# Kernel tuning notes

Measured on AMD Instinct MI355X. Metric: run time of the kernel, lower is better.

The kernel has to match this reference:

```python
import jax, jax.numpy as jnp
import numpy as np

N_NODES = 50000
N_EDGES = 800000
IN_DIM = 128
HID_DIM = 128
N_CLASSES = 40


def setup_inputs() -> dict:
    key = jax.random.key(0)
    ks = jax.random.split(key, 12)
    s = 0.05
    inp = {
        "X": jax.random.normal(ks[0], (N_NODES, IN_DIM), jnp.float32),
        "A": jax.random.randint(ks[1], (2, N_EDGES), 0, N_NODES, dtype=jnp.int64),
        "W0": jax.random.normal(ks[2], (HID_DIM, IN_DIM), jnp.float32) * s,
        "b0": jnp.zeros((HID_DIM,), jnp.float32),
        "W1": jax.random.normal(ks[3], (HID_DIM, HID_DIM), jnp.float32) * s,
        "b1": jnp.zeros((HID_DIM,), jnp.float32),
        "W2": jax.random.normal(ks[4], (HID_DIM, HID_DIM), jnp.float32) * s,
        "b2": jnp.zeros((HID_DIM,), jnp.float32),
        "W3": jax.random.normal(ks[5], (HID_DIM, HID_DIM), jnp.float32) * s,
        "b3": jnp.zeros((HID_DIM,), jnp.float32),
        "Wf": jax.random.normal(ks[6], (N_CLASSES, HID_DIM), jnp.float32) * s,
        "bf": jnp.zeros((N_CLASSES,), jnp.float32),
    }
    return inp


def _gcn_conv(x, W, b, src, dst):
    # FrobeniusNormGCNConv: normalize weight by Frobenius norm, then standard GCNConv
    Wn = W / jnp.linalg.norm(W)
    h = x @ Wn.T  # [N, out]
    # gcn_norm with self-loops (edge weight 1.0): deg over targets + 1 self loop
    ones = jnp.ones((dst.shape[0],), h.dtype)
    deg = jax.ops.segment_sum(ones, dst, num_segments=N_NODES) + 1.0
    dinv = jax.lax.rsqrt(deg)  # [N]
    norm = dinv[src] * dinv[dst]  # [E]
    # scatter-add of normalized source messages into targets
    agg = jax.ops.segment_sum(norm[:, None] * h[src], dst, num_segments=N_NODES)
    # self-loop contribution: dinv[i]^2 * h[i]; bias added after aggregation
    return agg + (dinv * dinv)[:, None] * h + b


def reference(X, A, W0, b0, W1, b1, W2, b2, W3, b3, Wf, bf):
    src, dst = A[0], A[1]
    h = _gcn_conv(X, W0, b0, src, dst)
    skip = h
    for W, b in ((W1, b1), (W2, b2), (W3, b3)):
        h = _gcn_conv(h, W, b, src, dst)
        h = jax.nn.relu(h)
        h = h + skip  # residual skip (dropout identity in eval mode)
        skip = h
    return h @ Wf.T + bf
```

## Files before the change

### kernel.cpp

```cpp
#include <hip/hip_runtime.h>

#define N_NODES_C 50000
#define N_EDGES_C 800000
#define DIM 128
#define NCLS 40
#define SCAN_NB ((N_NODES_C + 255) / 256)

typedef __attribute__((ext_vector_type(8))) short bf16x8;
typedef __attribute__((ext_vector_type(4))) float f32x4;

__device__ inline float bf2f(unsigned short u) {
    union { unsigned int i; float f; } c;
    c.i = ((unsigned int)u) << 16;
    return c.f;
}
__device__ inline unsigned short f2bf(float f) {
    union { float f; unsigned int i; } c;
    c.f = f;
    unsigned int x = c.i;
    x += 0x7fffu + ((x >> 16) & 1u);
    return (unsigned short)(x >> 16);
}
__device__ inline void add4b(float4& a, const ushort4& u) {
    a.x += bf2f(u.x);
    a.y += bf2f(u.y);
    a.z += bf2f(u.z);
    a.w += bf2f(u.w);
}

__global__ __launch_bounds__(256) void k_scales(const float* __restrict__ W0,
                                                const float* __restrict__ W1,
                                                const float* __restrict__ W2,
                                                const float* __restrict__ W3,
                                                float* __restrict__ scale_inv) {
    const float* W = blockIdx.x == 0 ? W0 : blockIdx.x == 1 ? W1 : blockIdx.x == 2 ? W2 : W3;
    float s = 0.f;
    for (int i = threadIdx.x; i < DIM * DIM; i += 256) {
        float v = W[i];
        s += v * v;
    }
    #pragma unroll
    for (int off = 32; off >= 1; off >>= 1) s += __shfl_down(s, off);
    __shared__ float red[4];
    int lane = threadIdx.x & 63, wid = threadIdx.x >> 6;
    if (lane == 0) red[wid] = s;
    __syncthreads();
    if (threadIdx.x == 0) {
        float tot = red[0] + red[1] + red[2] + red[3];
        scale_inv[blockIdx.x] = 1.0f / sqrtf(tot);
    }
}

__global__ __launch_bounds__(256) void k_f2b(const float* __restrict__ in,
                                             unsigned short* __restrict__ outb, int n4) {
    int i = blockIdx.x * 256 + threadIdx.x;
    if (i >= n4) return;
    float4 v = reinterpret_cast<const float4*>(in)[i];
    reinterpret_cast<ushort4*>(outb)[i] =
        make_ushort4(f2bf(v.x), f2bf(v.y), f2bf(v.z), f2bf(v.w));
}

__global__ __launch_bounds__(256) void k_w2b(const float* __restrict__ W0,
                                             const float* __restrict__ W1,
                                             const float* __restrict__ W2,
                                             const float* __restrict__ W3,
                                             unsigned short* __restrict__ Wb) {
    int m = blockIdx.x >> 4;
    int idx = (blockIdx.x & 15) * 256 + threadIdx.x;
    const float* W = m == 0 ? W0 : m == 1 ? W1 : m == 2 ? W2 : W3;
    float4 v = reinterpret_cast<const float4*>(W)[idx];
    reinterpret_cast<ushort4*>(Wb + (size_t)m * DIM * DIM)[idx] =
        make_ushort4(f2bf(v.x), f2bf(v.y), f2bf(v.z), f2bf(v.w));
}

__global__ void k_deg(const int* __restrict__ A, int* __restrict__ cnt, int E) {
    int e = blockIdx.x * 256 + threadIdx.x;
    if (e >= E) return;
    atomicAdd(&cnt[A[E + e]], 1);
}

__global__ __launch_bounds__(256) void k_scan_part(const int* __restrict__ cnt,
                                                   int* __restrict__ partial,
                                                   float* __restrict__ dinv, int n) {
    int idx = blockIdx.x * 256 + threadIdx.x;
    int v = (idx < n) ? cnt[idx] : 0;
    if (idx < n) dinv[idx] = rsqrtf((float)v + 1.0f);
    int s = v;
    #pragma unroll
    for (int off = 32; off >= 1; off >>= 1) s += __shfl_down(s, off);
    __shared__ int red[4];
    int lane = threadIdx.x & 63, wid = threadIdx.x >> 6;
    if (lane == 0) red[wid] = s;
    __syncthreads();
    if (threadIdx.x == 0) partial[blockIdx.x] = red[0] + red[1] + red[2] + red[3];
}

__global__ __launch_bounds__(256) void k_scan_mid(const int* __restrict__ partial,
                                                  int* __restrict__ base,
                                                  int* __restrict__ ptr, int nb, int n) {
    int tid = threadIdx.x;
    int v = (tid < nb) ? partial[tid] : 0;
    int lane = tid & 63, wid = tid >> 6;
    int sc = v;
    #pragma unroll
    for (int off = 1; off < 64; off <<= 1) {
        int t = __shfl_up(sc, off);
        if (lane >= off) sc += t;
    }
    __shared__ int wsum[4], wpre[4];
    if (lane == 63) wsum[wid] = sc;
    __syncthreads();
    if (tid == 0) {
        int acc = 0;
        #pragma unroll
        for (int w = 0; w < 4; ++w) { wpre[w] = acc; acc += wsum[w]; }
    }
    __syncthreads();
    int excl = wpre[wid] + sc - v;
    if (tid < nb) base[tid] = excl;
    if (tid == 255) ptr[n] = wpre[3] + sc;
}

__global__ __launch_bounds__(256) void k_scan_final(const int* __restrict__ cnt,
                                                    const int* __restrict__ base,
                                                    int* __restrict__ ptr, int n) {
    int idx = blockIdx.x * 256 + threadIdx.x;
    int v = (idx < n) ? cnt[idx] : 0;
    int tid = threadIdx.x, lane = tid & 63, wid = tid >> 6;
    int sc = v;
    #pragma unroll
    for (int off = 1; off < 64; off <<= 1) {
        int t = __shfl_up(sc, off);
        if (lane >= off) sc += t;
    }
    __shared__ int wsum[4], wpre[4];
    if (lane == 63) wsum[wid] = sc;
    __syncthreads();
    if (tid == 0) {
        int acc = 0;
        #pragma unroll
        for (int w = 0; w < 4; ++w) { wpre[w] = acc; acc += wsum[w]; }
    }
    __syncthreads();
    if (idx < n) ptr[idx] = base[blockIdx.x] + wpre[wid] + sc - v;
}

__global__ void k_fill(const int* __restrict__ A, const int* __restrict__ ptr,
                       int* __restrict__ fill, int* __restrict__ esrc, int E) {
    int e = blockIdx.x * 256 + threadIdx.x;
    if (e >= E) return;
    int s = A[e];
    int d = A[E + e];
    int pos = ptr[d] + atomicAdd(&fill[d], 1);
    esrc[pos] = s;
}

__global__ __launch_bounds__(256) void k_gemm_mfma(const unsigned short* __restrict__ Xb,
                                                   const unsigned short* __restrict__ Wb,
                                                   const float* __restrict__ scale_ptr,
                                                   const float* __restrict__ dinv,
                                                   unsigned short* __restrict__ Gb, int N) {
    int tid = threadIdx.x;
    int w = tid >> 6;
    int l = tid & 63;
    int l15 = l & 15;
    int lg = l >> 4;
    int arow = blockIdx.x * 64 + w * 16 + l15;
    if (arow >= N) arow = N - 1;
    float scale = scale_ptr[0];

    f32x4 acc[8];
    #pragma unroll
    for (int ct = 0; ct < 8; ++ct) acc[ct] = f32x4{0.f, 0.f, 0.f, 0.f};

    #pragma unroll
    for (int kc = 0; kc < 4; ++kc) {
        int ko = kc * 32 + lg * 8;
        bf16x8 a = *reinterpret_cast<const bf16x8*>(&Xb[(size_t)arow * DIM + ko]);
        #pragma unroll
        for (int ct = 0; ct < 8; ++ct) {
            bf16x8 b = *reinterpret_cast<const bf16x8*>(&Wb[(size_t)(ct * 16 + l15) * DIM + ko]);
            acc[ct] = __builtin_amdgcn_mfma_f32_16x16x32_bf16(a, b, acc[ct], 0, 0, 0);
        }
    }
    int outrow0 = blockIdx.x * 64 + w * 16 + lg * 4;
    #pragma unroll
    for (int r = 0; r < 4; ++r) {
        int row = outrow0 + r;
        if (row < N) {
            float dv = dinv[row] * scale;
            #pragma unroll
            for (int ct = 0; ct < 8; ++ct)
                Gb[(size_t)row * DIM + ct * 16 + l15] = f2bf(acc[ct][r] * dv);
        }
    }
}

__global__ __launch_bounds__(256) void k_agg(const unsigned short* __restrict__ Gb,
                                             const float* __restrict__ bias,
                                             const float* __restrict__ dinv,
                                             const int* __restrict__ ptr,
                                             const int* __restrict__ esrc,
                                             const unsigned short* __restrict__ skipb,
                                             unsigned short* __restrict__ outb,
                                             int relu_res, int N) {
    int n = blockIdx.x * 8 + (threadIdx.x >> 5);
    if (n >= N) return;
    int l = threadIdx.x & 31;
    const ushort4* __restrict__ Gv = reinterpret_cast<const ushort4*>(Gb);
    int beg = ptr[n], end = ptr[n + 1];
    float4 a0 = make_float4(0.f, 0.f, 0.f, 0.f), a1 = a0, a2 = a0, a3 = a0;
    int e = beg;
    for (; e + 8 <= end; e += 8) {
        int s0 = esrc[e + 0], s1 = esrc[e + 1], s2 = esrc[e + 2], s3 = esrc[e + 3];
        int s4 = esrc[e + 4], s5 = esrc[e + 5], s6 = esrc[e + 6], s7 = esrc[e + 7];
        ushort4 g0 = Gv[(size_t)s0 * 32 + l];
        ushort4 g1 = Gv[(size_t)s1 * 32 + l];
        ushort4 g2 = Gv[(size_t)s2 * 32 + l];
        ushort4 g3 = Gv[(size_t)s3 * 32 + l];
        ushort4 g4 = Gv[(size_t)s4 * 32 + l];
        ushort4 g5 = Gv[(size_t)s5 * 32 + l];
        ushort4 g6 = Gv[(size_t)s6 * 32 + l];
        ushort4 g7 = Gv[(size_t)s7 * 32 + l];
        add4b(a0, g0);
        add4b(a1, g1);
        add4b(a2, g2);
        add4b(a3, g3);
        add4b(a0, g4);
        add4b(a1, g5);
        add4b(a2, g6);
        add4b(a3, g7);
    }
    for (; e + 4 <= end; e += 4) {
        int s0 = esrc[e + 0], s1 = esrc[e + 1], s2 = esrc[e + 2], s3 = esrc[e + 3];
        ushort4 g0 = Gv[(size_t)s0 * 32 + l];
        ushort4 g1 = Gv[(size_t)s1 * 32 + l];
        ushort4 g2 = Gv[(size_t)s2 * 32 + l];
        ushort4 g3 = Gv[(size_t)s3 * 32 + l];
        add4b(a0, g0);
        add4b(a1, g1);
        add4b(a2, g2);
        add4b(a3, g3);
    }
    for (; e < end; ++e) {
        ushort4 g = Gv[(size_t)esrc[e] * 32 + l];
        add4b(a0, g);
    }
    float4 acc;
    acc.x = (a0.x + a1.x) + (a2.x + a3.x);
    acc.y = (a0.y + a1.y) + (a2.y + a3.y);
    acc.z = (a0.z + a1.z) + (a2.z + a3.z);
    acc.w = (a0.w + a1.w) + (a2.w + a3.w);

    float di = dinv[n];
    ushort4 gu = Gv[(size_t)n * 32 + l];
    float4 b4 = reinterpret_cast<const float4*>(bias)[l];
    float4 v;
    v.x = fmaf(di, acc.x + bf2f(gu.x), b4.x);
    v.y = fmaf(di, acc.y + bf2f(gu.y), b4.y);
    v.z = fmaf(di, acc.z + bf2f(gu.z), b4.z);
    v.w = fmaf(di, acc.w + bf2f(gu.w), b4.w);
    if (relu_res) {
        ushort4 su = reinterpret_cast<const ushort4*>(skipb)[(size_t)n * 32 + l];
        v.x = fmaxf(v.x, 0.f) + bf2f(su.x);
        v.y = fmaxf(v.y, 0.f) + bf2f(su.y);
        v.z = fmaxf(v.z, 0.f) + bf2f(su.z);
        v.w = fmaxf(v.w, 0.f) + bf2f(su.w);
    }
    reinterpret_cast<ushort4*>(outb)[(size_t)n * 32 + l] =
        make_ushort4(f2bf(v.x), f2bf(v.y), f2bf(v.z), f2bf(v.w));
}

__global__ __launch_bounds__(256) void k_final(const unsigned short* __restrict__ Hb,
                                               const float* __restrict__ Wf,
                                               const float* __restrict__ bf,
                                               float* __restrict__ out, int N) {
    __shared__ float Xs[16][68];
    __shared__ float Ws[16][64];
    int tid = threadIdx.x;
    int n0 = blockIdx.x * 64;
    int tx = tid & 15;
    int ty = tid >> 4;
    float acc[4][4] = {};
    for (int k0 = 0; k0 < DIM; k0 += 16) {
        {
            int j = tid >> 2, kq = tid & 3;
            int row = n0 + j;
            if (row >= N) row = N - 1;
            ushort4 x4 = *reinterpret_cast<const ushort4*>(&Hb[(size_t)row * DIM + k0 + kq * 4]);
            Xs[kq * 4 + 0][j] = bf2f(x4.x);
            Xs[kq * 4 + 1][j] = bf2f(x4.y);
            Xs[kq * 4 + 2][j] = bf2f(x4.z);
            Xs[kq * 4 + 3][j] = bf2f(x4.w);
        }
        {
            int o = tid >> 2, kq = tid & 3;
            int om = o < NCLS ? o : o - NCLS;
            const float4 w4 = *reinterpret_cast<const float4*>(&Wf[(size_t)om * DIM + k0 + kq * 4]);
            Ws[kq * 4 + 0][o] = w4.x;
            Ws[kq * 4 + 1][o] = w4.y;
            Ws[kq * 4 + 2][o] = w4.z;
            Ws[kq * 4 + 3][o] = w4.w;
        }
        __syncthreads();
        #pragma unroll
        for (int k = 0; k < 16; ++k) {
            float4 w = *reinterpret_cast<const float4*>(&Ws[k][tx * 4]);
            float4 x = *reinterpret_cast<const float4*>(&Xs[k][ty * 4]);
            float xv[4] = {x.x, x.y, x.z, x.w};
            #pragma unroll
            for (int i = 0; i < 4; ++i) {
                acc[i][0] = fmaf(xv[i], w.x, acc[i][0]);
                acc[i][1] = fmaf(xv[i], w.y, acc[i][1]);
                acc[i][2] = fmaf(xv[i], w.z, acc[i][2]);
                acc[i][3] = fmaf(xv[i], w.w, acc[i][3]);
            }
        }
        __syncthreads();
    }
    if (tx >= 10) return;
    float4 b4 = make_float4(bf[tx * 4], bf[tx * 4 + 1], bf[tx * 4 + 2], bf[tx * 4 + 3]);
    #pragma unroll
    for (int i = 0; i < 4; ++i) {
        int row = n0 + ty * 4 + i;
        if (row < N) {
            float* op = &out[(size_t)row * NCLS + tx * 4];
            op[0] = acc[i][0] + b4.x;
            op[1] = acc[i][1] + b4.y;
            op[2] = acc[i][2] + b4.z;
            op[3] = acc[i][3] + b4.w;
        }
    }
}

extern "C" void kernel_launch(void* const* d_in, const int* in_sizes, int n_in,
                              void* d_out, int out_size, void* d_ws, size_t ws_size,
                              hipStream_t stream) {
    (void)in_sizes; (void)n_in; (void)out_size; (void)ws_size;
    const float* X  = (const float*)d_in[0];
    const int*   A  = (const int*)d_in[1];
    const float* W0 = (const float*)d_in[2];
    const float* b0 = (const float*)d_in[3];
    const float* W1 = (const float*)d_in[4];
    const float* b1 = (const float*)d_in[5];
    const float* W2 = (const float*)d_in[6];
    const float* b2 = (const float*)d_in[7];
    const float* W3 = (const float*)d_in[8];
    const float* b3 = (const float*)d_in[9];
    const float* Wf = (const float*)d_in[10];
    const float* bf = (const float*)d_in[11];
    float* out = (float*)d_out;

    char* base_ws = (char*)d_ws;
    size_t off = 0;
    auto alloc = [&](size_t bytes) -> char* {
        char* p = base_ws + off;
        off = (off + bytes + 255) & ~(size_t)255;
        return p;
    };
    float* scale_inv = (float*)alloc(4 * sizeof(float));
    int*   deg   = (int*)alloc(N_NODES_C * sizeof(int));
    int*   fill  = (int*)alloc(N_NODES_C * sizeof(int));
    int*   ptr   = (int*)alloc((N_NODES_C + 1) * sizeof(int));
    float* dinv  = (float*)alloc(N_NODES_C * sizeof(float));
    int*   part  = (int*)alloc(SCAN_NB * sizeof(int));
    int*   bbase = (int*)alloc(SCAN_NB * sizeof(int));
    int*   esrc  = (int*)alloc((size_t)N_EDGES_C * sizeof(int));
    unsigned short* Gb  = (unsigned short*)alloc((size_t)N_NODES_C * DIM * sizeof(unsigned short));
    unsigned short* Xb  = (unsigned short*)alloc((size_t)N_NODES_C * DIM * sizeof(unsigned short));
    unsigned short* Hb1 = (unsigned short*)alloc((size_t)N_NODES_C * DIM * sizeof(unsigned short));
    unsigned short* Hb2 = (unsigned short*)alloc((size_t)N_NODES_C * DIM * sizeof(unsigned short));
    unsigned short* Wb  = (unsigned short*)alloc((size_t)4 * DIM * DIM * sizeof(unsigned short));

    hipMemsetAsync(deg, 0, N_NODES_C * sizeof(int), stream);
    hipMemsetAsync(fill, 0, N_NODES_C * sizeof(int), stream);

    k_scales<<<4, 256, 0, stream>>>(W0, W1, W2, W3, scale_inv);
    k_w2b<<<64, 256, 0, stream>>>(W0, W1, W2, W3, Wb);
    k_f2b<<<(N_NODES_C * DIM / 4 + 255) / 256, 256, 0, stream>>>(X, Xb, N_NODES_C * DIM / 4);
    k_deg<<<(N_EDGES_C + 255) / 256, 256, 0, stream>>>(A, deg, N_EDGES_C);
    k_scan_part<<<SCAN_NB, 256, 0, stream>>>(deg, part, dinv, N_NODES_C);
    k_scan_mid<<<1, 256, 0, stream>>>(part, bbase, ptr, SCAN_NB, N_NODES_C);
    k_scan_final<<<SCAN_NB, 256, 0, stream>>>(deg, bbase, ptr, N_NODES_C);
    k_fill<<<(N_EDGES_C + 255) / 256, 256, 0, stream>>>(A, ptr, fill, esrc, N_EDGES_C);

    const int gemm_grid = (N_NODES_C + 63) / 64;
    const int agg_grid  = (N_NODES_C + 7) / 8;

    k_gemm_mfma<<<gemm_grid, 256, 0, stream>>>(Xb, Wb + 0 * DIM * DIM, scale_inv + 0, dinv, Gb, N_NODES_C);
    k_agg<<<agg_grid, 256, 0, stream>>>(Gb, b0, dinv, ptr, esrc, nullptr, Hb1, 0, N_NODES_C);
    k_gemm_mfma<<<gemm_grid, 256, 0, stream>>>(Hb1, Wb + 1 * DIM * DIM, scale_inv + 1, dinv, Gb, N_NODES_C);
    k_agg<<<agg_grid, 256, 0, stream>>>(Gb, b1, dinv, ptr, esrc, Hb1, Hb2, 1, N_NODES_C);
    k_gemm_mfma<<<gemm_grid, 256, 0, stream>>>(Hb2, Wb + 2 * DIM * DIM, scale_inv + 2, dinv, Gb, N_NODES_C);
    k_agg<<<agg_grid, 256, 0, stream>>>(Gb, b2, dinv, ptr, esrc, Hb2, Hb1, 1, N_NODES_C);
    k_gemm_mfma<<<gemm_grid, 256, 0, stream>>>(Hb1, Wb + 3 * DIM * DIM, scale_inv + 3, dinv, Gb, N_NODES_C);
    k_agg<<<agg_grid, 256, 0, stream>>>(Gb, b3, dinv, ptr, esrc, Hb1, Hb2, 1, N_NODES_C);
    k_final<<<(N_NODES_C + 63) / 64, 256, 0, stream>>>(Hb2, Wf, bf, out, N_NODES_C);
}
```

Baseline: 364.1 us.

## Merge preprocessing kernels, fold scan middle pass, store edge sources as u16

Fuses the X/W bf16 conversion and weight-norm kernels into one launch. The fill-counter zeroing moves into the scan partial kernel, and the single-block middle scan is removed by having each final-scan block reduce the block partials itself. Edge source indices are stored as 16-bit values, which halves index traffic in the aggregation kernels. Node ids reach 49999, which exceeds the signed 16-bit range but fits in unsigned short, so the change is valid only while the node count stays below 65536.

```diff
diff --git a/kernel.cpp b/kernel.cpp
--- a/kernel.cpp
+++ b/kernel.cpp
@@ -5,6 +5,7 @@
 #define DIM 128
 #define NCLS 40
 #define SCAN_NB ((N_NODES_C + 255) / 256)
+#define F2B_NB ((N_NODES_C * DIM / 4) / 256)
 
 typedef __attribute__((ext_vector_type(8))) short bf16x8;
 typedef __attribute__((ext_vector_type(4))) float f32x4;
@@ -28,12 +29,34 @@
     a.w += bf2f(u.w);
 }
 
-__global__ __launch_bounds__(256) void k_scales(const float* __restrict__ W0,
-                                                const float* __restrict__ W1,
-                                                const float* __restrict__ W2,
-                                                const float* __restrict__ W3,
-                                                float* __restrict__ scale_inv) {
-    const float* W = blockIdx.x == 0 ? W0 : blockIdx.x == 1 ? W1 : blockIdx.x == 2 ? W2 : W3;
+__global__ __launch_bounds__(256) void k_pre(const float* __restrict__ X,
+                                             const float* __restrict__ W0,
+                                             const float* __restrict__ W1,
+                                             const float* __restrict__ W2,
+                                             const float* __restrict__ W3,
+                                             unsigned short* __restrict__ Xb,
+                                             unsigned short* __restrict__ Wb,
+                                             float* __restrict__ scale_inv) {
+    int b = blockIdx.x;
+    if (b < F2B_NB) {
+        int i = b * 256 + threadIdx.x;
+        float4 v = reinterpret_cast<const float4*>(X)[i];
+        reinterpret_cast<ushort4*>(Xb)[i] =
+            make_ushort4(f2bf(v.x), f2bf(v.y), f2bf(v.z), f2bf(v.w));
+        return;
+    }
+    b -= F2B_NB;
+    if (b < 64) {
+        int m = b >> 4;
+        int idx = (b & 15) * 256 + threadIdx.x;
+        const float* W = m == 0 ? W0 : m == 1 ? W1 : m == 2 ? W2 : W3;
+        float4 v = reinterpret_cast<const float4*>(W)[idx];
+        reinterpret_cast<ushort4*>(Wb + (size_t)m * DIM * DIM)[idx] =
+            make_ushort4(f2bf(v.x), f2bf(v.y), f2bf(v.z), f2bf(v.w));
+        return;
+    }
+    b -= 64;
+    const float* W = b == 0 ? W0 : b == 1 ? W1 : b == 2 ? W2 : W3;
     float s = 0.f;
     for (int i = threadIdx.x; i < DIM * DIM; i += 256) {
         float v = W[i];
@@ -47,30 +70,8 @@
     __syncthreads();
     if (threadIdx.x == 0) {
         float tot = red[0] + red[1] + red[2] + red[3];
-        scale_inv[blockIdx.x] = 1.0f / sqrtf(tot);
-    }
-}
-
-__global__ __launch_bounds__(256) void k_f2b(const float* __restrict__ in,
-                                             unsigned short* __restrict__ outb, int n4) {
-    int i = blockIdx.x * 256 + threadIdx.x;
-    if (i >= n4) return;
-    float4 v = reinterpret_cast<const float4*>(in)[i];
-    reinterpret_cast<ushort4*>(outb)[i] =
-        make_ushort4(f2bf(v.x), f2bf(v.y), f2bf(v.z), f2bf(v.w));
-}
-
-__global__ __launch_bounds__(256) void k_w2b(const float* __restrict__ W0,
-                                             const float* __restrict__ W1,
-                                             const float* __restrict__ W2,
-                                             const float* __restrict__ W3,
-                                             unsigned short* __restrict__ Wb) {
-    int m = blockIdx.x >> 4;
-    int idx = (blockIdx.x & 15) * 256 + threadIdx.x;
-    const float* W = m == 0 ? W0 : m == 1 ? W1 : m == 2 ? W2 : W3;
-    float4 v = reinterpret_cast<const float4*>(W)[idx];
-    reinterpret_cast<ushort4*>(Wb + (size_t)m * DIM * DIM)[idx] =
-        make_ushort4(f2bf(v.x), f2bf(v.y), f2bf(v.z), f2bf(v.w));
+        scale_inv[b] = 1.0f / sqrtf(tot);
+    }
 }
 
 __global__ void k_deg(const int* __restrict__ A, int* __restrict__ cnt, int E) {
@@ -81,10 +82,14 @@
 
 __global__ __launch_bounds__(256) void k_scan_part(const int* __restrict__ cnt,
                                                    int* __restrict__ partial,
-                                                   float* __restrict__ dinv, int n) {
+                                                   float* __restrict__ dinv,
+                                                   int* __restrict__ fill, int n) {
     int idx = blockIdx.x * 256 + threadIdx.x;
     int v = (idx < n) ? cnt[idx] : 0;
-    if (idx < n) dinv[idx] = rsqrtf((float)v + 1.0f);
+    if (idx < n) {
+        dinv[idx] = rsqrtf((float)v + 1.0f);
+        fill[idx] = 0;
+    }
     int s = v;
     #pragma unroll
     for (int off = 32; off >= 1; off >>= 1) s += __shfl_down(s, off);
@@ -95,12 +100,30 @@
     if (threadIdx.x == 0) partial[blockIdx.x] = red[0] + red[1] + red[2] + red[3];
 }
 
-__global__ __launch_bounds__(256) void k_scan_mid(const int* __restrict__ partial,
-                                                  int* __restrict__ base,
-                                                  int* __restrict__ ptr, int nb, int n) {
-    int tid = threadIdx.x;
-    int v = (tid < nb) ? partial[tid] : 0;
+__global__ __launch_bounds__(256) void k_scan_final(const int* __restrict__ cnt,
+                                                    const int* __restrict__ partial,
+                                                    int* __restrict__ ptr, int n, int nb) {
+    int tid = threadIdx.x, bid = blockIdx.x;
     int lane = tid & 63, wid = tid >> 6;
+    int pv = (tid < nb) ? partial[tid] : 0;
+    int vb = (tid < bid) ? pv : 0;
+    int s1 = vb, s2 = pv;
+    #pragma unroll
+    for (int off = 32; off >= 1; off >>= 1) {
+        s1 += __shfl_down(s1, off);
+        s2 += __shfl_down(s2, off);
+    }
+    __shared__ int r1[4], r2[4];
+    if (lane == 0) { r1[wid] = s1; r2[wid] = s2; }
+    __syncthreads();
+    __shared__ int sbase, stot;
+    if (tid == 0) {
+        sbase = r1[0] + r1[1] + r1[2] + r1[3];
+        stot  = r2[0] + r2[1] + r2[2] + r2[3];
+    }
+    __syncthreads();
+    int idx = bid * 256 + tid;
+    int v = (idx < n) ? cnt[idx] : 0;
     int sc = v;
     #pragma unroll
     for (int off = 1; off < 64; off <<= 1) {
@@ -116,43 +139,18 @@
         for (int w = 0; w < 4; ++w) { wpre[w] = acc; acc += wsum[w]; }
     }
     __syncthreads();
-    int excl = wpre[wid] + sc - v;
-    if (tid < nb) base[tid] = excl;
-    if (tid == 255) ptr[n] = wpre[3] + sc;
-}
-
-__global__ __launch_bounds__(256) void k_scan_final(const int* __restrict__ cnt,
-                                                    const int* __restrict__ base,
-                                                    int* __restrict__ ptr, int n) {
-    int idx = blockIdx.x * 256 + threadIdx.x;
-    int v = (idx < n) ? cnt[idx] : 0;
-    int tid = threadIdx.x, lane = tid & 63, wid = tid >> 6;
-    int sc = v;
-    #pragma unroll
-    for (int off = 1; off < 64; off <<= 1) {
-        int t = __shfl_up(sc, off);
-        if (lane >= off) sc += t;
-    }
-    __shared__ int wsum[4], wpre[4];
-    if (lane == 63) wsum[wid] = sc;
-    __syncthreads();
-    if (tid == 0) {
-        int acc = 0;
-        #pragma unroll
-        for (int w = 0; w < 4; ++w) { wpre[w] = acc; acc += wsum[w]; }
-    }
-    __syncthreads();
-    if (idx < n) ptr[idx] = base[blockIdx.x] + wpre[wid] + sc - v;
+    if (idx < n) ptr[idx] = sbase + wpre[wid] + sc - v;
+    if (bid == 0 && tid == 0) ptr[n] = stot;
 }
 
 __global__ void k_fill(const int* __restrict__ A, const int* __restrict__ ptr,
-                       int* __restrict__ fill, int* __restrict__ esrc, int E) {
+                       int* __restrict__ fill, unsigned short* __restrict__ esrc, int E) {
     int e = blockIdx.x * 256 + threadIdx.x;
     if (e >= E) return;
     int s = A[e];
     int d = A[E + e];
     int pos = ptr[d] + atomicAdd(&fill[d], 1);
-    esrc[pos] = s;
+    esrc[pos] = (unsigned short)s;
 }
 
 __global__ __launch_bounds__(256) void k_gemm_mfma(const unsigned short* __restrict__ Xb,
@@ -200,7 +198,7 @@
                                              const float* __restrict__ bias,
                                              const float* __restrict__ dinv,
                                              const int* __restrict__ ptr,
-                                             const int* __restrict__ esrc,
+                                             const unsigned short* __restrict__ esrc,
                                              const unsigned short* __restrict__ skipb,
                                              unsigned short* __restrict__ outb,
                                              int relu_res, int N) {
@@ -364,8 +362,7 @@
     int*   ptr   = (int*)alloc((N_NODES_C + 1) * sizeof(int));
     float* dinv  = (float*)alloc(N_NODES_C * sizeof(float));
     int*   part  = (int*)alloc(SCAN_NB * sizeof(int));
-    int*   bbase = (int*)alloc(SCAN_NB * sizeof(int));
-    int*   esrc  = (int*)alloc((size_t)N_EDGES_C * sizeof(int));
+    unsigned short* esrc = (unsigned short*)alloc((size_t)N_EDGES_C * sizeof(unsigned short));
     unsigned short* Gb  = (unsigned short*)alloc((size_t)N_NODES_C * DIM * sizeof(unsigned short));
     unsigned short* Xb  = (unsigned short*)alloc((size_t)N_NODES_C * DIM * sizeof(unsigned short));
     unsigned short* Hb1 = (unsigned short*)alloc((size_t)N_NODES_C * DIM * sizeof(unsigned short));
@@ -373,15 +370,11 @@
     unsigned short* Wb  = (unsigned short*)alloc((size_t)4 * DIM * DIM * sizeof(unsigned short));
 
     hipMemsetAsync(deg, 0, N_NODES_C * sizeof(int), stream);
-    hipMemsetAsync(fill, 0, N_NODES_C * sizeof(int), stream);
-
-    k_scales<<<4, 256, 0, stream>>>(W0, W1, W2, W3, scale_inv);
-    k_w2b<<<64, 256, 0, stream>>>(W0, W1, W2, W3, Wb);
-    k_f2b<<<(N_NODES_C * DIM / 4 + 255) / 256, 256, 0, stream>>>(X, Xb, N_NODES_C * DIM / 4);
+
+    k_pre<<<F2B_NB + 64 + 4, 256, 0, stream>>>(X, W0, W1, W2, W3, Xb, Wb, scale_inv);
     k_deg<<<(N_EDGES_C + 255) / 256, 256, 0, stream>>>(A, deg, N_EDGES_C);
-    k_scan_part<<<SCAN_NB, 256, 0, stream>>>(deg, part, dinv, N_NODES_C);
-    k_scan_mid<<<1, 256, 0, stream>>>(part, bbase, ptr, SCAN_NB, N_NODES_C);
-    k_scan_final<<<SCAN_NB, 256, 0, stream>>>(deg, bbase, ptr, N_NODES_C);
+    k_scan_part<<<SCAN_NB, 256, 0, stream>>>(deg, part, dinv, fill, N_NODES_C);
+    k_scan_final<<<SCAN_NB, 256, 0, stream>>>(deg, part, ptr, N_NODES_C, SCAN_NB);
     k_fill<<<(N_EDGES_C + 255) / 256, 256, 0, stream>>>(A, ptr, fill, esrc, N_EDGES_C);
 
     const int gemm_grid = (N_NODES_C + 63) / 64;
```

Result: faster. 348.7 us (-4.2%).
